# Performance work log

Measured on AMD Instinct MI355X. Metric: run time of the kernel, lower is better.

## Reference

```python
import jax, jax.numpy as jnp
import numpy as np

# Static architecture dims (match init_kwargs)
B, T, NB, SX, SY = 1, 10, 10, 1200, 1200
ND, NS, DIV = 5, 5, 4            # dynamic bands, static bands, pool size
OX = OY = SX // DIV + 2          # 302 (conv pad1 -> pool floor -> conv pad1)
FLAT = NB * OX * OY              # 912040
PW = ((SX + 2) // DIV) * DIV     # 1200: maxpool floor-mode coverage of the 1202-wide map


def setup_inputs() -> dict:
    key = jax.random.key(0)
    ks = jax.random.split(key, 17)
    n = lambda k, s, sc=1.0: jax.random.normal(k, s, dtype=jnp.float32) * sc
    return {
        "x": n(ks[0], (B, T, NB, SX, SY)),
        "conv1_w": n(ks[1], (2 * NB, NB), 0.1),   # 1x1 conv as (out_c, in_c)
        "conv1_b": n(ks[2], (2 * NB,), 0.1),
        "conv2_w": n(ks[3], (NB, 2 * NB), 0.1),
        "conv2_b": n(ks[4], (NB,), 0.1),
        "w_ih": n(ks[5], (ND, 4), 0.5),           # per-band LSTM, gates i,f,g,o (H=1, in=1)
        "w_hh": n(ks[6], (ND, 4), 0.5),
        "b_ih": n(ks[7], (ND, 4), 0.5),
        "b_hh": n(ks[8], (ND, 4), 0.5),
        "fc1_w": n(ks[9], (64, FLAT), 0.001),
        "fc1_b": n(ks[10], (64,)),
        "fc2_w": n(ks[11], (64, 64), 0.1),
        "fc2_b": n(ks[12], (64,)),
        "fc3_w": n(ks[13], (16, 64), 0.1),
        "fc3_b": n(ks[14], (16,)),
        "fc4_w": n(ks[15], (3, 16), 0.1),
        "fc4_b": n(ks[16], (3,)),
    }


def _forward(x, conv1_w, conv1_b, conv2_w, conv2_b, w_ih, w_hh, b_ih, b_hh,
             fc1_w, fc1_b, fc2_w, fc2_b, fc3_w, fc3_b, fc4_w, fc4_b):
    xf = x.reshape(B * T, NB, SX, SY)
    # Conv2d(k=1, pad=1): zero-pad input ring then 1x1 conv + bias -> (BT, 2NB, 1202, 1202)
    xp = jnp.pad(xf, ((0, 0), (0, 0), (1, 1), (1, 1)))
    h = jnp.einsum('bcxy,oc->boxy', xp, conv1_w) + conv1_b[None, :, None, None]
    # MaxPool2d(k=4, s=4), floor mode: drop remainder cols/rows, reshape-max
    NW = PW // DIV  # 300
    h = h[:, :, :PW, :PW].reshape(B * T, 2 * NB, NW, DIV, NW, DIV).max(axis=(3, 5))
    # Second Conv2d(k=1, pad=1) -> (BT, NB, 302, 302)
    hp = jnp.pad(h, ((0, 0), (0, 0), (1, 1), (1, 1)))
    h = jnp.einsum('bcxy,oc->boxy', hp, conv2_w) + conv2_b[None, :, None, None]
    x5 = h.reshape(B, T, NB, OX, OY)
    dyn = x5[:, :, :ND]      # bandas_time = [0..4]
    stat = x5[:, -1, ND:]    # (B, NS, OX, OY)
    # Faithful to torch .view: raw row-major reinterpretation (B,T,ND,OX,OY) -> (B*OX*OY, T, ND)
    xd = dyn.reshape(B * OX * OY, T, ND)
    bias = (b_ih + b_hh)[None]  # (1, ND, 4)

    def step(carry, xt):
        hh, cc = carry  # each (PB, ND)
        g = xt[:, :, None] * w_ih[None] + hh[:, :, None] * w_hh[None] + bias
        i = jax.nn.sigmoid(g[..., 0])
        f = jax.nn.sigmoid(g[..., 1])
        gg = jnp.tanh(g[..., 2])
        o = jax.nn.sigmoid(g[..., 3])
        cc = f * cc + i * gg
        hh = o * jnp.tanh(cc)
        return (hh, cc), None

    z = jnp.zeros((B * OX * OY, ND), jnp.float32)
    (hT, _), _ = jax.lax.scan(step, (z, z), jnp.transpose(xd, (1, 0, 2)))
    x_dyn = hT.reshape(B, OX, OY, ND).transpose(0, 3, 1, 2)  # (B, ND, OX, OY)
    feat = jnp.concatenate([x_dyn, stat], axis=1).reshape(B, FLAT)
    y = feat @ fc1_w.T + fc1_b
    y = y @ fc2_w.T + fc2_b
    y = jax.nn.relu(y)
    y = y @ fc3_w.T + fc3_b
    y = y @ fc4_w.T + fc4_b
    return y


def reference(x, conv1_w, conv1_b, conv2_w, conv2_b, w_ih, w_hh, b_ih, b_hh,
              fc1_w, fc1_b, fc2_w, fc2_b, fc3_w, fc3_b, fc4_w, fc4_b):
    return _forward(x, conv1_w, conv1_b, conv2_w, conv2_b, w_ih, w_hh, b_ih, b_hh,
                    fc1_w, fc1_b, fc2_w, fc2_b, fc3_w, fc3_b, fc4_w, fc4_b)
```

## Files before the change

kernel.cpp:

```cpp
#include <hip/hip_runtime.h>
#include <math.h>

#define T_    10
#define NB_   10
#define C1_   20
#define SX_   1200
#define OX_   302
#define S2_   (OX_*OX_)
#define NP_   300
#define ND_   5
#define FLAT_ (NB_*S2_)
#define XBLK_FC1 446

typedef float f4 __attribute__((ext_vector_type(4)));
typedef float f2 __attribute__((ext_vector_type(2)));

__global__ __launch_bounds__(256, 4) void k_convpool(const float* __restrict__ x,
                                                     const float* __restrict__ w1,
                                                     const float* __restrict__ b1,
                                                     const float* __restrict__ w2,
                                                     const float* __restrict__ b2,
                                                     float* __restrict__ dynb,
                                                     float* __restrict__ feat) {
    const int t = blockIdx.z;
    if (t == T_) {
        int s = (blockIdx.y * 5 + blockIdx.x) * 256 + threadIdx.y * 64 + threadIdx.x;
        if (s >= S2_) return;
        int ox = s / OX_, oy = s % OX_;
        if (ox != 0 && ox != OX_ - 1 && oy != 0 && oy != OX_ - 1) return;
#pragma unroll
        for (int d = 0; d < ND_; ++d) {
            float v = b2[d];
#pragma unroll
            for (int tt = 0; tt < T_; ++tt) dynb[(tt * ND_ + d) * S2_ + s] = v;
        }
#pragma unroll
        for (int c = 0; c < ND_; ++c) feat[(ND_ + c) * S2_ + s] = b2[ND_ + c];
        return;
    }

    const int lane  = threadIdx.x;
    const int obase = blockIdx.x * 63;
    const int px    = blockIdx.y * 4 + threadIdx.y;

    const int lc  = 4 * (obase - 1 + lane);
    const int lcc = lc < 0 ? 0 : (lc > SX_ - 4 ? SX_ - 4 : lc);
    const bool m3valid = (lc >= 0);

    float pool012[C1_], pool3[C1_];
#pragma unroll
    for (int o = 0; o < C1_; ++o) { pool012[o] = -3.0e38f; pool3[o] = -3.0e38f; }

    const int rs = (px > 0) ? 4 * px - 1 : 0;
    const int re = 4 * px + 2;
    const float* xt = x + (size_t)t * NB_ * SX_ * SX_;
    const f2* w1p = (const f2*)w1;

    for (int row = rs; row <= re; ++row) {
        f4 xq[NB_];
#pragma unroll
        for (int c = 0; c < NB_; ++c)
            xq[c] = *(const f4*)(xt + ((size_t)c * SX_ + row) * SX_ + lcc);
        f2 x01[NB_], x23[NB_];
#pragma unroll
        for (int c = 0; c < NB_; ++c) {
            x01[c] = __builtin_shufflevector(xq[c], xq[c], 0, 1);
            x23[c] = __builtin_shufflevector(xq[c], xq[c], 2, 3);
        }
#pragma unroll
        for (int o = 0; o < C1_; ++o) {
            f2 h01, h23;
            {
                f2 w = w1p[o * 5 + 0];
                asm("v_pk_mul_f32 %0, %1, %2 op_sel:[0,0] op_sel_hi:[1,0]"
                    : "=v"(h01) : "v"(x01[0]), "s"(w));
                asm("v_pk_mul_f32 %0, %1, %2 op_sel:[0,0] op_sel_hi:[1,0]"
                    : "=v"(h23) : "v"(x23[0]), "s"(w));
                asm("v_pk_fma_f32 %0, %1, %2, %0 op_sel:[0,1,0] op_sel_hi:[1,1,1]"
                    : "+v"(h01) : "v"(x01[1]), "s"(w));
                asm("v_pk_fma_f32 %0, %1, %2, %0 op_sel:[0,1,0] op_sel_hi:[1,1,1]"
                    : "+v"(h23) : "v"(x23[1]), "s"(w));
            }
#pragma unroll
            for (int c2 = 1; c2 < 5; ++c2) {
                f2 w = w1p[o * 5 + c2];
                asm("v_pk_fma_f32 %0, %1, %2, %0 op_sel:[0,0,0] op_sel_hi:[1,0,1]"
                    : "+v"(h01) : "v"(x01[2 * c2]), "s"(w));
                asm("v_pk_fma_f32 %0, %1, %2, %0 op_sel:[0,0,0] op_sel_hi:[1,0,1]"
                    : "+v"(h23) : "v"(x23[2 * c2]), "s"(w));
                asm("v_pk_fma_f32 %0, %1, %2, %0 op_sel:[0,1,0] op_sel_hi:[1,1,1]"
                    : "+v"(h01) : "v"(x01[2 * c2 + 1]), "s"(w));
                asm("v_pk_fma_f32 %0, %1, %2, %0 op_sel:[0,1,0] op_sel_hi:[1,1,1]"
                    : "+v"(h23) : "v"(x23[2 * c2 + 1]), "s"(w));
            }
            pool012[o] = fmaxf(pool012[o], fmaxf(fmaxf(h01.x, h01.y), h23.x));
            pool3[o]   = fmaxf(pool3[o], h23.y);
        }
    }

    const int py = obase + lane;
    const bool edge = (px == 0) | (py == 0);
    float pool[C1_];
#pragma unroll
    for (int o = 0; o < C1_; ++o) {
        float m3    = m3valid ? pool3[o] : -3.0e38f;
        float other = __shfl_down(pool012[o], 1, 64);
        float p = fmaxf(m3, other);
        if (edge) p = fmaxf(p, 0.f);
        pool[o] = p + b1[o];
    }

    if (lane < 63 && py < NP_) {
        int s = (px + 1) * OX_ + (py + 1);
        float out[NB_];
#pragma unroll
        for (int o2 = 0; o2 < NB_; ++o2) {
            float a = b2[o2];
#pragma unroll
            for (int o = 0; o < C1_; ++o) a = fmaf(w2[o2 * C1_ + o], pool[o], a);
            out[o2] = a;
        }
#pragma unroll
        for (int d = 0; d < ND_; ++d) dynb[(t * ND_ + d) * S2_ + s] = out[d];
        if (t == T_ - 1) {
#pragma unroll
            for (int c = 0; c < ND_; ++c) feat[(ND_ + c) * S2_ + s] = out[ND_ + c];
        }
    }
}

__global__ __launch_bounds__(256) void k_lstm(const float* __restrict__ dynb,
                                              const float* __restrict__ w_ih,
                                              const float* __restrict__ w_hh,
                                              const float* __restrict__ b_ih,
                                              const float* __restrict__ b_hh,
                                              float* __restrict__ feat) {
    int i = blockIdx.x * 256 + threadIdx.x;
    if (i >= S2_ * ND_) return;
    int p = i / ND_, d = i - p * ND_;

    float wi[4], wh[4], bb[4];
#pragma unroll
    for (int g = 0; g < 4; ++g) {
        wi[g] = w_ih[d * 4 + g];
        wh[g] = w_hh[d * 4 + g];
        bb[g] = b_ih[d * 4 + g] + b_hh[d * 4 + g];
    }
    float h = 0.f, cc = 0.f;
#pragma unroll 1
    for (int tt = 0; tt < T_; ++tt) {
        float xt = dynb[p * (T_ * ND_) + tt * ND_ + d];
        float g0 = fmaf(xt, wi[0], fmaf(h, wh[0], bb[0]));
        float g1 = fmaf(xt, wi[1], fmaf(h, wh[1], bb[1]));
        float g2 = fmaf(xt, wi[2], fmaf(h, wh[2], bb[2]));
        float g3 = fmaf(xt, wi[3], fmaf(h, wh[3], bb[3]));
        float ig = __builtin_amdgcn_rcpf(1.f + __expf(-g0));
        float fg = __builtin_amdgcn_rcpf(1.f + __expf(-g1));
        float gg = fmaf(2.f, __builtin_amdgcn_rcpf(1.f + __expf(-2.f * g2)), -1.f);
        float og = __builtin_amdgcn_rcpf(1.f + __expf(-g3));
        cc = fg * cc + ig * gg;
        float th = fmaf(2.f, __builtin_amdgcn_rcpf(1.f + __expf(-2.f * cc)), -1.f);
        h = og * th;
    }
    feat[d * S2_ + p] = h;
}

__global__ __launch_bounds__(256) void k_fc1(const float* __restrict__ feat,
                                             const float* __restrict__ w,
                                             float* __restrict__ partial) {
    __shared__ float red[4][32];
    const int tid = threadIdx.x;
    const int jbase = blockIdx.y * 32;
    const int NI4 = FLAT_ / 4;
    const int HALF = XBLK_FC1 * 256;
    float acc[32];
#pragma unroll
    for (int j = 0; j < 32; ++j) acc[j] = 0.f;
    const float* wb = w + (size_t)jbase * FLAT_;

    int i4a = blockIdx.x * 256 + tid;
    int i4b = i4a + HALF;
    {
        f4 f = *(const f4*)(feat + (size_t)i4a * 4);
#pragma unroll
        for (int j = 0; j < 32; ++j) {
            f4 wv = *(const f4*)(wb + (size_t)j * FLAT_ + (size_t)i4a * 4);
            acc[j] = fmaf(wv.x, f.x, acc[j]);
            acc[j] = fmaf(wv.y, f.y, acc[j]);
            acc[j] = fmaf(wv.z, f.z, acc[j]);
            acc[j] = fmaf(wv.w, f.w, acc[j]);
        }
    }
    if (i4b < NI4) {
        f4 f = *(const f4*)(feat + (size_t)i4b * 4);
#pragma unroll
        for (int j = 0; j < 32; ++j) {
            f4 wv = *(const f4*)(wb + (size_t)j * FLAT_ + (size_t)i4b * 4);
            acc[j] = fmaf(wv.x, f.x, acc[j]);
            acc[j] = fmaf(wv.y, f.y, acc[j]);
            acc[j] = fmaf(wv.z, f.z, acc[j]);
            acc[j] = fmaf(wv.w, f.w, acc[j]);
        }
    }
    int lane = tid & 63, wid = tid >> 6;
#pragma unroll
    for (int j = 0; j < 32; ++j) {
        float v = acc[j];
#pragma unroll
        for (int off = 32; off >= 1; off >>= 1) v += __shfl_xor(v, off, 64);
        if (lane == 0) red[wid][j] = v;
    }
    __syncthreads();
    if (tid < 32) {
        float s = red[0][tid] + red[1][tid] + red[2][tid] + red[3][tid];
        partial[blockIdx.x * 64 + jbase + tid] = s;
    }
}

__global__ __launch_bounds__(256) void k_head(const float* __restrict__ partial,
                                              const float* __restrict__ fc1_b,
                                              const float* __restrict__ fc2_w,
                                              const float* __restrict__ fc2_b,
                                              const float* __restrict__ fc3_w,
                                              const float* __restrict__ fc3_b,
                                              const float* __restrict__ fc4_w,
                                              const float* __restrict__ fc4_b,
                                              float* __restrict__ out) {
    __shared__ float r4[256];
    __shared__ float y1[64], y2[64], y3[16];
    int tid = threadIdx.x;
    int j = tid & 63, q = tid >> 6;
    float s = 0.f;
    for (int b = q; b < XBLK_FC1; b += 4) s += partial[b * 64 + j];
    r4[tid] = s;
    __syncthreads();
    if (tid < 64)
        y1[tid] = r4[tid] + r4[64 + tid] + r4[128 + tid] + r4[192 + tid] + fc1_b[tid];
    __syncthreads();
    if (tid < 64) {
        float a = fc2_b[tid];
#pragma unroll
        for (int k = 0; k < 64; ++k) a = fmaf(fc2_w[tid * 64 + k], y1[k], a);
        y2[tid] = fmaxf(a, 0.f);
    }
    __syncthreads();
    if (tid < 16) {
        float a = fc3_b[tid];
#pragma unroll
        for (int k = 0; k < 64; ++k) a = fmaf(fc3_w[tid * 64 + k], y2[k], a);
        y3[tid] = a;
    }
    __syncthreads();
    if (tid < 3) {
        float a = fc4_b[tid];
#pragma unroll
        for (int k = 0; k < 16; ++k) a = fmaf(fc4_w[tid * 16 + k], y3[k], a);
        out[tid] = a;
    }
}

extern "C" void kernel_launch(void* const* d_in, const int* in_sizes, int n_in,
                              void* d_out, int out_size, void* d_ws, size_t ws_size,
                              hipStream_t stream) {
    const float* x     = (const float*)d_in[0];
    const float* w1    = (const float*)d_in[1];
    const float* b1    = (const float*)d_in[2];
    const float* w2    = (const float*)d_in[3];
    const float* b2    = (const float*)d_in[4];
    const float* w_ih  = (const float*)d_in[5];
    const float* w_hh  = (const float*)d_in[6];
    const float* b_ih  = (const float*)d_in[7];
    const float* b_hh  = (const float*)d_in[8];
    const float* fc1_w = (const float*)d_in[9];
    const float* fc1_b = (const float*)d_in[10];
    const float* fc2_w = (const float*)d_in[11];
    const float* fc2_b = (const float*)d_in[12];
    const float* fc3_w = (const float*)d_in[13];
    const float* fc3_b = (const float*)d_in[14];
    const float* fc4_w = (const float*)d_in[15];
    const float* fc4_b = (const float*)d_in[16];

    float* ws      = (float*)d_ws;
    float* dynb    = ws;
    float* feat    = ws + (size_t)T_ * ND_ * S2_;
    float* partial = feat + FLAT_;

    hipLaunchKernelGGL(k_convpool, dim3(5, 75, T_ + 1), dim3(64, 4), 0, stream,
                       x, w1, b1, w2, b2, dynb, feat);
    hipLaunchKernelGGL(k_lstm, dim3((S2_ * ND_ + 255) / 256), dim3(256), 0, stream,
                       dynb, w_ih, w_hh, b_ih, b_hh, feat);
    hipLaunchKernelGGL(k_fc1, dim3(XBLK_FC1, 2), dim3(256), 0, stream,
                       feat, fc1_w, partial);
    hipLaunchKernelGGL(k_head, dim3(1), dim3(256), 0, stream,
                       partial, fc1_b, fc2_w, fc2_b, fc3_w, fc3_b, fc4_w, fc4_b,
                       (float*)d_out);
}
```

Before: 215.8 us.

## Split conv1 output channels across two wavefronts and combine through shared memory

The conv+pool kernel now gives each pooled pixel row to two wavefronts. Each wavefront computes 10 of the 20 conv1 output channels, and the grid is doubled in y to keep coverage. The partial pooled values go through shared memory, and one wavefront finishes the second 1x1 conv over all 20 channels. The aim is to cut per-thread register pressure and serial FMA work and so raise occupancy and parallelism. In exchange, each input row is now loaded by two wavefronts instead of one, and the kernel gains a block-wide barrier.

After: 335.5 us. 55.5% more time.

```diff
diff --git a/kernel.cpp b/kernel.cpp
--- a/kernel.cpp
+++ b/kernel.cpp
@@ -39,22 +39,29 @@
         return;
     }
 
-    const int lane  = threadIdx.x;
-    const int obase = blockIdx.x * 63;
-    const int px    = blockIdx.y * 4 + threadIdx.y;
+    __shared__ float smem[2][2][64][11];
+
+    const int lane   = threadIdx.x;
+    const int ty     = threadIdx.y;
+    const int px_sub = ty >> 1;
+    const int chh    = ty & 1;
+    const int ch     = chh * 10;
+    const int obase  = blockIdx.x * 63;
+    const int px     = blockIdx.y * 2 + px_sub;
 
     const int lc  = 4 * (obase - 1 + lane);
     const int lcc = lc < 0 ? 0 : (lc > SX_ - 4 ? SX_ - 4 : lc);
     const bool m3valid = (lc >= 0);
 
-    float pool012[C1_], pool3[C1_];
-#pragma unroll
-    for (int o = 0; o < C1_; ++o) { pool012[o] = -3.0e38f; pool3[o] = -3.0e38f; }
+    const float* xt = x + (size_t)t * NB_ * SX_ * SX_;
+    const f2* w1p = (const f2*)w1 + ch * 5;
+
+    float pool012[10], pool3[10];
+#pragma unroll
+    for (int o = 0; o < 10; ++o) { pool012[o] = -3.0e38f; pool3[o] = -3.0e38f; }
 
     const int rs = (px > 0) ? 4 * px - 1 : 0;
     const int re = 4 * px + 2;
-    const float* xt = x + (size_t)t * NB_ * SX_ * SX_;
-    const f2* w1p = (const f2*)w1;
 
     for (int row = rs; row <= re; ++row) {
         f4 xq[NB_];
@@ -68,7 +75,7 @@
             x23[c] = __builtin_shufflevector(xq[c], xq[c], 2, 3);
         }
 #pragma unroll
-        for (int o = 0; o < C1_; ++o) {
+        for (int o = 0; o < 10; ++o) {
             f2 h01, h23;
             {
                 f2 w = w1p[o * 5 + 0];
@@ -100,24 +107,33 @@
 
     const int py = obase + lane;
     const bool edge = (px == 0) | (py == 0);
-    float pool[C1_];
-#pragma unroll
-    for (int o = 0; o < C1_; ++o) {
+    float pool[10];
+#pragma unroll
+    for (int o = 0; o < 10; ++o) {
         float m3    = m3valid ? pool3[o] : -3.0e38f;
         float other = __shfl_down(pool012[o], 1, 64);
         float p = fmaxf(m3, other);
         if (edge) p = fmaxf(p, 0.f);
-        pool[o] = p + b1[o];
-    }
-
-    if (lane < 63 && py < NP_) {
+        pool[o] = p + b1[ch + o];
+    }
+
+#pragma unroll
+    for (int o = 0; o < 10; ++o) smem[px_sub][chh][lane][o] = pool[o];
+    __syncthreads();
+
+    if (chh == 0 && lane < 63 && py < NP_) {
+        float pb[10];
+#pragma unroll
+        for (int o = 0; o < 10; ++o) pb[o] = smem[px_sub][1][lane][o];
         int s = (px + 1) * OX_ + (py + 1);
         float out[NB_];
 #pragma unroll
         for (int o2 = 0; o2 < NB_; ++o2) {
             float a = b2[o2];
 #pragma unroll
-            for (int o = 0; o < C1_; ++o) a = fmaf(w2[o2 * C1_ + o], pool[o], a);
+            for (int o = 0; o < 10; ++o) a = fmaf(w2[o2 * C1_ + o], pool[o], a);
+#pragma unroll
+            for (int o = 0; o < 10; ++o) a = fmaf(w2[o2 * C1_ + 10 + o], pb[o], a);
             out[o2] = a;
         }
 #pragma unroll
@@ -285,7 +301,7 @@
     float* feat    = ws + (size_t)T_ * ND_ * S2_;
     float* partial = feat + FLAT_;
 
-    hipLaunchKernelGGL(k_convpool, dim3(5, 75, T_ + 1), dim3(64, 4), 0, stream,
+    hipLaunchKernelGGL(k_convpool, dim3(5, 150, T_ + 1), dim3(64, 4), 0, stream,
                        x, w1, b1, w2, b2, dynb, feat);
     hipLaunchKernelGGL(k_lstm, dim3((S2_ * ND_ + 255) / 256), dim3(256), 0, stream,
                        dynb, w_ih, w_hh, b_ih, b_hh, feat);
```
